# Optimization experiments

Measured on AMD Instinct MI355X. Metric: run time of the kernel, lower is better.

The kernel has to match this reference:

```python
import jax, jax.numpy as jnp
import numpy as np

N = 30000
E = 480000
D = 128
H = 3  # n_hop
BN_EPS = 1e-5


def _bn(x, g, b, m, v):
    # inference-mode BatchNorm1d
    return (x - m) * jax.lax.rsqrt(v + BN_EPS) * g + b


def setup_inputs() -> dict:
    key = jax.random.key(0)
    ks = jax.random.split(key, 16)
    inp = {
        "xs": jax.random.normal(ks[0], (H + 1, N, D), dtype=jnp.float32),
        "ei": jax.random.randint(ks[1], (H, 2, E), 0, N, dtype=jnp.int32),
        "lW1": jax.random.normal(ks[2], (D, D), dtype=jnp.float32) * 0.05,
        "lb1": jnp.zeros((D,), jnp.float32),
        "lg": jax.random.uniform(ks[3], (D,), jnp.float32, 0.5, 1.5),
        "lbt": jax.random.normal(ks[4], (D,), dtype=jnp.float32) * 0.1,
        "lm": jax.random.normal(ks[5], (D,), dtype=jnp.float32) * 0.1,
        "lv": jax.random.uniform(ks[6], (D,), jnp.float32, 0.5, 1.5),
        "lW2": jax.random.normal(ks[7], (D, D), dtype=jnp.float32) * 0.05,
        "lb2": jnp.zeros((D,), jnp.float32),
        "eps": jnp.zeros((H,), jnp.float32),
        "cW1": jax.random.normal(ks[8], (H, D, D), dtype=jnp.float32) * 0.05,
        "cb1": jnp.zeros((H, D), jnp.float32),
        "cg": jax.random.uniform(ks[9], (H, D), jnp.float32, 0.5, 1.5),
        "cbt": jax.random.normal(ks[10], (H, D), dtype=jnp.float32) * 0.1,
        "cm": jax.random.normal(ks[11], (H, D), dtype=jnp.float32) * 0.1,
        "cv": jax.random.uniform(ks[12], (H, D), jnp.float32, 0.5, 1.5),
        "cW2": jax.random.normal(ks[13], (H, D, D), dtype=jnp.float32) * 0.05,
        "cb2": jnp.zeros((H, D), jnp.float32),
    }
    return inp


def reference(xs, ei, lW1, lb1, lg, lbt, lm, lv, lW2, lb2,
              eps, cW1, cb1, cg, cbt, cm, cv, cW2, cb2):
    # self.lin: Linear -> BN -> ReLU -> Linear on multi_input[0]
    h0 = jax.nn.relu(_bn(xs[0] @ lW1 + lb1, lg, lbt, lm, lv)) @ lW2 + lb2
    hidden = h0  # dropout identity (eval)
    for k in range(H):
        x = xs[k + 1]                       # [N, D]
        src, dst = ei[k, 0], ei[k, 1]
        agg = jax.ops.segment_sum(x[src], dst, num_segments=N)  # sum_{j->i} x_j
        z = (1.0 + eps[k]) * x + agg        # GIN update
        prop = jax.nn.relu(_bn(z @ cW1[k] + cb1[k], cg[k], cbt[k], cm[k], cv[k])) @ cW2[k] + cb2[k]
        hidden = hidden + prop
    return hidden
```

## Files before the change

kernel.cpp:

```cpp
#include <hip/hip_runtime.h>

#define N_NODES 30000
#define N_EDGES 480000
#define D 128
#define H 3
#define BN_EPS 1e-5f
#define M_TOT (H * N_NODES)
#define E_TOT (H * N_EDGES)

#define NCH 64
#define CHE (N_EDGES / NCH)
#define NBKT 512
#define NBKT_TOT (H * NBKT)
#define CELLS (NBKT_TOT * NCH)
#define SCAN_NBLK (CELLS / 1024)
#define CONV_N4 (3 * N_NODES * D / 4)
#define CONV_BLK ((CONV_N4 + 255) / 256)
#define TILES ((N_NODES + 63) / 64)
#define PREP_FIX (H * NCH + 9)

typedef __attribute__((ext_vector_type(8))) short short8v;
typedef __attribute__((ext_vector_type(4))) float f32x4;

__device__ __forceinline__ ushort f2bf(float f) {
    uint u = __float_as_uint(f);
    u += 0x7fffu + ((u >> 16) & 1u);
    return (ushort)(u >> 16);
}
__device__ __forceinline__ float bf2f(ushort b) {
    return __uint_as_float(((uint)b) << 16);
}

#define DOT2(accv, w, msk) \
    asm("v_dot2_f32_bf16 %0, %1, %2, %0" : "+v"(accv) : "v"(w), "v"(msk))

__global__ __launch_bounds__(256) void prep_k(
    const float* __restrict__ xs, const int* __restrict__ ei,
    const float* __restrict__ lW1, const float* __restrict__ lW2,
    const float* __restrict__ cW1, const float* __restrict__ cW2,
    const float* __restrict__ lb1, const float* __restrict__ lg,
    const float* __restrict__ lbt, const float* __restrict__ lm,
    const float* __restrict__ lv,
    const float* __restrict__ cb1, const float* __restrict__ cg,
    const float* __restrict__ cbt, const float* __restrict__ cm,
    const float* __restrict__ cv,
    const float* __restrict__ lb2, const float* __restrict__ cb2,
    ushort* __restrict__ Wt, float* __restrict__ scof,
    ushort* __restrict__ xball, int* __restrict__ cnts)
{
    const int bid = blockIdx.x;
    const int tid = threadIdx.x;
    if (bid < H * NCH) {
        __shared__ int hc[NBKT];
        const int hop = bid >> 6, c = bid & 63;
        for (int i = tid; i < NBKT; i += 256) hc[i] = 0;
        __syncthreads();
        const int* dstp = ei + (size_t)hop * 2 * N_EDGES + N_EDGES + c * CHE;
        for (int i = tid; i < CHE; i += 256)
            atomicAdd(&hc[dstp[i] >> 6], 1);
        __syncthreads();
        for (int b = tid; b < NBKT; b += 256)
            cnts[((hop * NBKT + b) << 6) | c] = hc[b];
    } else if (bid < H * NCH + 8) {
        const int mat = bid - H * NCH;
        const float* src;
        if (mat == 0) src = lW1;
        else if (mat == 1) src = lW2;
        else {
            const int k = (mat - 2) >> 1;
            src = ((mat & 1) == 0 ? cW1 : cW2) + (size_t)k * D * D;
        }
        ushort* dst = Wt + (size_t)mat * D * D;
        for (int idx = tid; idx < D * D; idx += 256) {
            const int n = idx >> 7, k = idx & 127;
            dst[idx] = f2bf(src[k * D + n]);
        }
    } else if (bid == H * NCH + 8) {
        for (int t = tid; t < 512; t += 256) {
            const int L = t >> 7, c = t & 127;
            float g, v, b, m, bt;
            if (L == 0) { g = lg[c]; v = lv[c]; b = lb1[c]; m = lm[c]; bt = lbt[c]; }
            else {
                const int k = L - 1;
                g = cg[k * D + c]; v = cv[k * D + c]; b = cb1[k * D + c];
                m = cm[k * D + c]; bt = cbt[k * D + c];
            }
            const float s = g * rsqrtf(v + BN_EPS);
            scof[L * 256 + c] = s;
            scof[L * 256 + 128 + c] = (b - m) * s + bt;
        }
        if (tid < 128) {
            float t = lb2[tid];
            for (int k = 0; k < H; ++k) t += cb2[k * D + tid];
            scof[1024 + tid] = t;
        }
    } else {
        const int i = (bid - PREP_FIX) * 256 + tid;
        if (i < CONV_N4) {
            const float4 v = ((const float4*)(xs + (size_t)N_NODES * D))[i];
            ushort4 o;
            o.x = f2bf(v.x); o.y = f2bf(v.y); o.z = f2bf(v.z); o.w = f2bf(v.w);
            ((ushort4*)(xball + (size_t)N_NODES * D))[i] = o;
        }
    }
}

#define LW 136

__global__ __launch_bounds__(256) void layerpar_k(
    const float* __restrict__ xs0, const ushort* __restrict__ zb,
    const ushort* __restrict__ Wt, const float* __restrict__ scof,
    ushort* __restrict__ parts)
{
    __shared__ ushort Xs[64 * LW];
    __shared__ ushort Ws[128 * LW];
    const int L = blockIdx.x & 3, tile = blockIdx.x >> 2;
    const int row0 = tile * 64;
    const int tid = threadIdx.x;
    const int wave = tid >> 6, lane = tid & 63;
    const int m16 = lane & 15, kq = lane >> 4;

    const ushort* W1t = Wt + (size_t)(2 * L) * D * D;
    const ushort* W2t = W1t + D * D;
    const float* scL = scof + L * 256;

    if (L == 0) {
        for (int f = tid; f < 2048; f += 256) {
            const int r = f >> 5, c4 = (f & 31) << 2;
            const int gr = row0 + r;
            ushort4 v = make_ushort4(0, 0, 0, 0);
            if (gr < N_NODES) {
                const float4 fv = *(const float4*)(xs0 + (size_t)gr * D + c4);
                v.x = f2bf(fv.x); v.y = f2bf(fv.y);
                v.z = f2bf(fv.z); v.w = f2bf(fv.w);
            }
            *(ushort4*)(&Xs[r * LW + c4]) = v;
        }
    } else {
        const ushort* X = zb + (size_t)(L - 1) * N_NODES * D;
        for (int f = tid; f < 2048; f += 256) {
            const int r = f >> 5, c4 = (f & 31) << 2;
            const int gr = row0 + r;
            ushort4 v = make_ushort4(0, 0, 0, 0);
            if (gr < N_NODES) v = *(const ushort4*)(X + (size_t)gr * D + c4);
            *(ushort4*)(&Xs[r * LW + c4]) = v;
        }
    }
    for (int f = tid; f < 4096; f += 256) {
        const int n = f >> 5, c4 = (f & 31) << 2;
        *(ushort4*)(&Ws[n * LW + c4]) = *(const ushort4*)(W1t + n * D + c4);
    }
    __syncthreads();

    const int arow = wave * 16 + m16;
    short8v a[4];
#pragma unroll
    for (int kk = 0; kk < 4; ++kk)
        a[kk] = *(const short8v*)(&Xs[arow * LW + kk * 32 + kq * 8]);

    f32x4 acc[8];
#pragma unroll
    for (int t = 0; t < 8; ++t) acc[t] = (f32x4){0.f, 0.f, 0.f, 0.f};
#pragma unroll
    for (int kk = 0; kk < 4; ++kk) {
#pragma unroll
        for (int t = 0; t < 8; ++t) {
            const short8v b = *(const short8v*)(&Ws[(t * 16 + m16) * LW + kk * 32 + kq * 8]);
            acc[t] = __builtin_amdgcn_mfma_f32_16x16x32_bf16(a[kk], b, acc[t], 0, 0, 0);
        }
    }
    __syncthreads();

#pragma unroll
    for (int t = 0; t < 8; ++t) {
        const int n = t * 16 + m16;
        const float sc = scL[n], of = scL[128 + n];
#pragma unroll
        for (int r = 0; r < 4; ++r)
            Xs[(wave * 16 + kq * 4 + r) * LW + n] = f2bf(fmaxf(acc[t][r] * sc + of, 0.f));
    }
    for (int f = tid; f < 4096; f += 256) {
        const int n = f >> 5, c4 = (f & 31) << 2;
        *(ushort4*)(&Ws[n * LW + c4]) = *(const ushort4*)(W2t + n * D + c4);
    }
    __syncthreads();

    short8v ah[4];
#pragma unroll
    for (int kk = 0; kk < 4; ++kk)
        ah[kk] = *(const short8v*)(&Xs[arow * LW + kk * 32 + kq * 8]);
    f32x4 accO[8];
#pragma unroll
    for (int t = 0; t < 8; ++t) accO[t] = (f32x4){0.f, 0.f, 0.f, 0.f};
#pragma unroll
    for (int kk = 0; kk < 4; ++kk) {
#pragma unroll
        for (int t = 0; t < 8; ++t) {
            const short8v b = *(const short8v*)(&Ws[(t * 16 + m16) * LW + kk * 32 + kq * 8]);
            accO[t] = __builtin_amdgcn_mfma_f32_16x16x32_bf16(ah[kk], b, accO[t], 0, 0, 0);
        }
    }

    ushort* pL = parts + (size_t)L * N_NODES * D;
#pragma unroll
    for (int t = 0; t < 8; ++t) {
        const int n = t * 16 + m16;
#pragma unroll
        for (int r = 0; r < 4; ++r) {
            const int gr = row0 + wave * 16 + kq * 4 + r;
            if (gr < N_NODES) pL[(size_t)gr * D + n] = f2bf(accO[t][r]);
        }
    }
}

__global__ __launch_bounds__(256) void reduce_k(const ushort* __restrict__ parts,
                                                const float* __restrict__ scof,
                                                float* __restrict__ out)
{
    const int i = blockIdx.x * 256 + threadIdx.x;
    const size_t LS = (size_t)N_NODES * D / 4;
    const uint2* pp = (const uint2*)parts;
    const uint2 q0 = pp[i];
    const uint2 q1 = pp[i + LS];
    const uint2 q2 = pp[i + 2 * LS];
    const uint2 q3 = pp[i + 3 * LS];
    const float4 bb = ((const float4*)(scof + 1024))[i & 31];
    float4 s;
    s.x = ((bf2f((ushort)(q0.x & 0xffff)) + bf2f((ushort)(q1.x & 0xffff))) +
           (bf2f((ushort)(q2.x & 0xffff)) + bf2f((ushort)(q3.x & 0xffff)))) + bb.x;
    s.y = ((bf2f((ushort)(q0.x >> 16)) + bf2f((ushort)(q1.x >> 16))) +
           (bf2f((ushort)(q2.x >> 16)) + bf2f((ushort)(q3.x >> 16)))) + bb.y;
    s.z = ((bf2f((ushort)(q0.y & 0xffff)) + bf2f((ushort)(q1.y & 0xffff))) +
           (bf2f((ushort)(q2.y & 0xffff)) + bf2f((ushort)(q3.y & 0xffff)))) + bb.z;
    s.w = ((bf2f((ushort)(q0.y >> 16)) + bf2f((ushort)(q1.y >> 16))) +
           (bf2f((ushort)(q2.y >> 16)) + bf2f((ushort)(q3.y >> 16)))) + bb.w;
    ((float4*)out)[i] = s;
}

__global__ __launch_bounds__(1024) void scanA_k(int* __restrict__ cnts,
                                                int* __restrict__ bsums) {
    __shared__ int sh[1024];
    const int tid = threadIdx.x;
    const int i = blockIdx.x * 1024 + tid;
    const int v = cnts[i];
    sh[tid] = v;
    __syncthreads();
    int val = v;
    for (int off = 1; off < 1024; off <<= 1) {
        const int t = (tid >= off) ? sh[tid - off] : 0;
        __syncthreads();
        val += t;
        sh[tid] = val;
        __syncthreads();
    }
    cnts[i] = val - v;
    if (tid == 1023) bsums[blockIdx.x] = val;
}

__global__ __launch_bounds__(1024) void scanC_k(int* __restrict__ cnts,
                                                const int* __restrict__ bsums,
                                                int* __restrict__ offs) {
    __shared__ int bs[128];
    const int tid = threadIdx.x;
    if (tid < 128) bs[tid] = (tid < SCAN_NBLK) ? bsums[tid] : 0;
    __syncthreads();
    for (int off = 1; off < 128; off <<= 1) {
        int t = 0;
        if (tid < 128 && tid >= off) t = bs[tid - off];
        __syncthreads();
        if (tid < 128) bs[tid] += t;
        __syncthreads();
    }
    const int add = (blockIdx.x == 0) ? 0 : bs[blockIdx.x - 1];
    const int i = blockIdx.x * 1024 + tid;
    cnts[i] += add;
    if (i == 0) offs[M_TOT] = E_TOT;
}

__global__ __launch_bounds__(256) void binplace_k(const int* __restrict__ ei,
                                                  const int* __restrict__ cnts,
                                                  uint* __restrict__ binned) {
    __shared__ int cur[NBKT];
    const int chunk = blockIdx.x;
    const int hop = chunk >> 6, c = chunk & 63;
    for (int b = threadIdx.x; b < NBKT; b += 256)
        cur[b] = cnts[((hop * NBKT + b) << 6) | c];
    __syncthreads();
    const int* srcp = ei + (size_t)hop * 2 * N_EDGES + c * CHE;
    const int* dstp = srcp + N_EDGES;
    for (int i = threadIdx.x; i < CHE; i += 256) {
        const int s = srcp[i], d = dstp[i];
        const int slot = atomicAdd(&cur[d >> 6], 1);
        binned[slot] = ((uint)(d & 63) << 16) | (uint)s;
    }
}

__global__ __launch_bounds__(256) void cat_k(const uint* __restrict__ binned,
                                             const int* __restrict__ cnts,
                                             int* __restrict__ offs,
                                             ushort* __restrict__ srcs) {
    const int B = blockIdx.x;
    const int hop = B >> 9, bb = B & 511;
    const int dstbase = bb << 6;
    if (dstbase >= N_NODES) return;
    const int bB = cnts[B << 6];
    const int bE = (B == NBKT_TOT - 1) ? E_TOT : cnts[(B + 1) << 6];
    const int cnt = bE - bB;

    __shared__ uint ent[2048];
    __shared__ ushort stg[2048];
    __shared__ int hist[64], cur[64];

    for (int d = threadIdx.x; d < 64; d += 256) hist[d] = 0;
    __syncthreads();
    for (int i = threadIdx.x; i < cnt; i += 256) {
        const uint e = binned[bB + i];
        ent[i] = e;
        atomicAdd(&hist[e >> 16], 1);
    }
    __syncthreads();
    if (threadIdx.x < 64) {
        const int v = hist[threadIdx.x];
        int x = v;
        for (int off = 1; off < 64; off <<= 1) {
            const int t = __shfl_up(x, off, 64);
            if (threadIdx.x >= off) x += t;
        }
        cur[threadIdx.x] = x - v;
        const int gd = dstbase + threadIdx.x;
        if (gd < N_NODES) offs[hop * N_NODES + gd] = bB + x - v;
    }
    __syncthreads();
    for (int i = threadIdx.x; i < cnt; i += 256) {
        const uint e = ent[i];
        const int lp = atomicAdd(&cur[e >> 16], 1);
        stg[lp] = (ushort)(e & 0xffffu);
    }
    __syncthreads();
    for (int i = threadIdx.x; i < cnt; i += 256)
        srcs[bB + i] = stg[i];
}

__global__ __launch_bounds__(256) void agg_k(const ushort* __restrict__ xball,
                                             const int* __restrict__ offs,
                                             const ushort* __restrict__ srcs,
                                             const float* __restrict__ eps,
                                             ushort* __restrict__ zb) {
    const int gnode = blockIdx.x * 4 + (threadIdx.x >> 6);
    const int hop = gnode / N_NODES;
    const int node = gnode - hop * N_NODES;
    const int lane = threadIdx.x & 63;
    const int eh = lane >> 4;
    const int cl = lane & 15;
    const float a = 1.0f + eps[hop];
    const char* xb = (const char*)(xball + (size_t)(hop + 1) * N_NODES * D);
    const uint coff = (uint)cl << 4;
    const uint MLO = 0x00003F80u;
    const uint MHI = 0x3F800000u;

    float acc[8];
#pragma unroll
    for (int q = 0; q < 8; ++q) acc[q] = 0.f;
    if (eh == 0) {
        const uint4 sv = *(const uint4*)(xb + (((uint)node << 8) + coff));
        const uint w[4] = {sv.x, sv.y, sv.z, sv.w};
#pragma unroll
        for (int q = 0; q < 4; ++q) {
            acc[2 * q]     = a * bf2f((ushort)(w[q] & 0xffff));
            acc[2 * q + 1] = a * bf2f((ushort)(w[q] >> 16));
        }
    }

    const int beg = offs[gnode], end = offs[gnode + 1];
    for (int i = beg; i < end; i += 32) {
        uint4 v[8];
#pragma unroll
        for (int u = 0; u < 8; ++u) {
            const int p = i + u * 4 + eh;
            v[u] = make_uint4(0u, 0u, 0u, 0u);
            if (p < end) {
                const uint boff = ((uint)srcs[p] << 8) + coff;
                v[u] = *(const uint4*)(xb + boff);
            }
        }
#pragma unroll
        for (int u = 0; u < 8; ++u) {
            DOT2(acc[0], v[u].x, MLO); DOT2(acc[1], v[u].x, MHI);
            DOT2(acc[2], v[u].y, MLO); DOT2(acc[3], v[u].y, MHI);
            DOT2(acc[4], v[u].z, MLO); DOT2(acc[5], v[u].z, MHI);
            DOT2(acc[6], v[u].w, MLO); DOT2(acc[7], v[u].w, MHI);
        }
    }
#pragma unroll
    for (int q = 0; q < 8; ++q) {
        acc[q] += __shfl_xor(acc[q], 16);
        acc[q] += __shfl_xor(acc[q], 32);
    }
    if (eh == 0) {
        uint4 o;
        o.x = (uint)f2bf(acc[0]) | ((uint)f2bf(acc[1]) << 16);
        o.y = (uint)f2bf(acc[2]) | ((uint)f2bf(acc[3]) << 16);
        o.z = (uint)f2bf(acc[4]) | ((uint)f2bf(acc[5]) << 16);
        o.w = (uint)f2bf(acc[6]) | ((uint)f2bf(acc[7]) << 16);
        ((uint4*)zb)[(size_t)gnode * 16 + cl] = o;
    }
}

extern "C" void kernel_launch(void* const* d_in, const int* in_sizes, int n_in,
                              void* d_out, int out_size, void* d_ws, size_t ws_size,
                              hipStream_t stream)
{
    const float* xs  = (const float*)d_in[0];
    const int*   ei  = (const int*)d_in[1];
    const float* lW1 = (const float*)d_in[2];
    const float* lb1 = (const float*)d_in[3];
    const float* lg  = (const float*)d_in[4];
    const float* lbt = (const float*)d_in[5];
    const float* lm  = (const float*)d_in[6];
    const float* lv  = (const float*)d_in[7];
    const float* lW2 = (const float*)d_in[8];
    const float* lb2 = (const float*)d_in[9];
    const float* eps = (const float*)d_in[10];
    const float* cW1 = (const float*)d_in[11];
    const float* cb1 = (const float*)d_in[12];
    const float* cg  = (const float*)d_in[13];
    const float* cbt = (const float*)d_in[14];
    const float* cm  = (const float*)d_in[15];
    const float* cv  = (const float*)d_in[16];
    const float* cW2 = (const float*)d_in[17];
    const float* cb2 = (const float*)d_in[18];
    float* out = (float*)d_out;

    char* ws = (char*)d_ws;
    ushort* xball = (ushort*)ws; ws += (size_t)4 * N_NODES * D * sizeof(ushort);
    ushort* zb    = (ushort*)ws; ws += (size_t)H * N_NODES * D * sizeof(ushort);
    ushort* parts = (ushort*)ws; ws += (size_t)4 * N_NODES * D * sizeof(ushort);
    ushort* Wt    = (ushort*)ws; ws += (size_t)8 * D * D * sizeof(ushort);
    float*  scof  = (float*)ws;  ws += (size_t)(4 * 256 + 128) * sizeof(float);
    int* cnts     = (int*)ws;    ws += (size_t)CELLS * sizeof(int);
    int* bsums    = (int*)ws;    ws += 128 * sizeof(int);
    int* offs     = (int*)ws;    ws += (size_t)(M_TOT + 64) * sizeof(int);
    uint* binned  = (uint*)ws;   ws += (size_t)E_TOT * sizeof(uint);
    ushort* srcs  = (ushort*)ws;

    prep_k<<<PREP_FIX + CONV_BLK, 256, 0, stream>>>(
        xs, ei, lW1, lW2, cW1, cW2, lb1, lg, lbt, lm, lv,
        cb1, cg, cbt, cm, cv, lb2, cb2, Wt, scof, xball, cnts);

    scanA_k<<<SCAN_NBLK, 1024, 0, stream>>>(cnts, bsums);
    scanC_k<<<SCAN_NBLK, 1024, 0, stream>>>(cnts, bsums, offs);
    binplace_k<<<H * NCH, 256, 0, stream>>>(ei, cnts, binned);
    cat_k<<<NBKT_TOT, 256, 0, stream>>>(binned, cnts, offs, srcs);

    agg_k<<<M_TOT / 4, 256, 0, stream>>>(xball, offs, srcs, eps, zb);
    layerpar_k<<<TILES * 4, 256, 0, stream>>>(xs, zb, Wt, scof, parts);
    reduce_k<<<(N_NODES * D / 4) / 256, 256, 0, stream>>>(parts, scof, out);
}
```

Before: 155.6 us.

## Fuse second-layer GEMMs into one K=512 GEMM replacing partial sums and reduce

The four per-layer second linear layers and the reduction kernel are replaced by one concatenated GEMM. The hidden activations of all four branches are stored side by side as an [N,512] bf16 matrix, and the W2 matrices are concatenated along K, so a single GEMM with the combined bias gives the output directly. This removes the bf16 partial buffers, their extra rounding and the separate reduce pass. The first GEMM kernel also drops LDS staging and reads operands straight from global memory, which saves barriers but relies on cache hits for the repeated W1 fragment loads.

Result: slower. 187.5 us (+20.5%).

```diff
diff --git a/kernel.cpp b/kernel.cpp
--- a/kernel.cpp
+++ b/kernel.cpp
@@ -17,7 +17,8 @@
 #define CONV_N4 (3 * N_NODES * D / 4)
 #define CONV_BLK ((CONV_N4 + 255) / 256)
 #define TILES ((N_NODES + 63) / 64)
-#define PREP_FIX (H * NCH + 9)
+#define PREP_FIX (H * NCH + 13)
+#define DK 512
 
 typedef __attribute__((ext_vector_type(8))) short short8v;
 typedef __attribute__((ext_vector_type(4))) float f32x4;
@@ -46,7 +47,8 @@
     const float* __restrict__ cv,
     const float* __restrict__ lb2, const float* __restrict__ cb2,
     ushort* __restrict__ Wt, float* __restrict__ scof,
-    ushort* __restrict__ xball, int* __restrict__ cnts)
+    ushort* __restrict__ xball, int* __restrict__ cnts,
+    ushort* __restrict__ W2c)
 {
     const int bid = blockIdx.x;
     const int tid = threadIdx.x;
@@ -94,6 +96,13 @@
             for (int k = 0; k < H; ++k) t += cb2[k * D + tid];
             scof[1024 + tid] = t;
         }
+    } else if (bid < H * NCH + 13) {
+        const int L = bid - (H * NCH + 9);
+        const float* src = (L == 0) ? lW2 : cW2 + (size_t)(L - 1) * D * D;
+        for (int idx = tid; idx < D * D; idx += 256) {
+            const int n = idx >> 7, k = idx & 127;
+            W2c[(size_t)n * DK + L * D + k] = f2bf(src[k * D + n]);
+        }
     } else {
         const int i = (bid - PREP_FIX) * 256 + tid;
         if (i < CONV_N4) {
@@ -105,136 +114,116 @@
     }
 }
 
-#define LW 136
-
-__global__ __launch_bounds__(256) void layerpar_k(
+__global__ __launch_bounds__(256) void hgen_k(
     const float* __restrict__ xs0, const ushort* __restrict__ zb,
     const ushort* __restrict__ Wt, const float* __restrict__ scof,
-    ushort* __restrict__ parts)
+    ushort* __restrict__ Hm)
 {
-    __shared__ ushort Xs[64 * LW];
-    __shared__ ushort Ws[128 * LW];
     const int L = blockIdx.x & 3, tile = blockIdx.x >> 2;
-    const int row0 = tile * 64;
-    const int tid = threadIdx.x;
-    const int wave = tid >> 6, lane = tid & 63;
+    const int wave = threadIdx.x >> 6, lane = threadIdx.x & 63;
     const int m16 = lane & 15, kq = lane >> 4;
+    const int rbase = tile * 64 + wave * 16;
+    const int arow = rbase + m16;
 
     const ushort* W1t = Wt + (size_t)(2 * L) * D * D;
-    const ushort* W2t = W1t + D * D;
     const float* scL = scof + L * 256;
 
+    short8v a[4];
     if (L == 0) {
-        for (int f = tid; f < 2048; f += 256) {
-            const int r = f >> 5, c4 = (f & 31) << 2;
-            const int gr = row0 + r;
-            ushort4 v = make_ushort4(0, 0, 0, 0);
-            if (gr < N_NODES) {
-                const float4 fv = *(const float4*)(xs0 + (size_t)gr * D + c4);
-                v.x = f2bf(fv.x); v.y = f2bf(fv.y);
-                v.z = f2bf(fv.z); v.w = f2bf(fv.w);
+        if (arow < N_NODES) {
+            const float* xp = xs0 + (size_t)arow * D + kq * 8;
+#pragma unroll
+            for (int kk = 0; kk < 4; ++kk) {
+                const float4 f0 = *(const float4*)(xp + kk * 32);
+                const float4 f1 = *(const float4*)(xp + kk * 32 + 4);
+                short8v av;
+                av[0] = (short)f2bf(f0.x); av[1] = (short)f2bf(f0.y);
+                av[2] = (short)f2bf(f0.z); av[3] = (short)f2bf(f0.w);
+                av[4] = (short)f2bf(f1.x); av[5] = (short)f2bf(f1.y);
+                av[6] = (short)f2bf(f1.z); av[7] = (short)f2bf(f1.w);
+                a[kk] = av;
             }
-            *(ushort4*)(&Xs[r * LW + c4]) = v;
+        } else {
+#pragma unroll
+            for (int kk = 0; kk < 4; ++kk) a[kk] = (short8v)(short)0;
         }
     } else {
-        const ushort* X = zb + (size_t)(L - 1) * N_NODES * D;
-        for (int f = tid; f < 2048; f += 256) {
-            const int r = f >> 5, c4 = (f & 31) << 2;
-            const int gr = row0 + r;
-            ushort4 v = make_ushort4(0, 0, 0, 0);
-            if (gr < N_NODES) v = *(const ushort4*)(X + (size_t)gr * D + c4);
-            *(ushort4*)(&Xs[r * LW + c4]) = v;
-        }
-    }
-    for (int f = tid; f < 4096; f += 256) {
-        const int n = f >> 5, c4 = (f & 31) << 2;
-        *(ushort4*)(&Ws[n * LW + c4]) = *(const ushort4*)(W1t + n * D + c4);
-    }
-    __syncthreads();
-
-    const int arow = wave * 16 + m16;
-    short8v a[4];
-#pragma unroll
-    for (int kk = 0; kk < 4; ++kk)
-        a[kk] = *(const short8v*)(&Xs[arow * LW + kk * 32 + kq * 8]);
+        if (arow < N_NODES) {
+            const ushort* xp = zb + (size_t)(L - 1) * N_NODES * D
+                                  + (size_t)arow * D + kq * 8;
+#pragma unroll
+            for (int kk = 0; kk < 4; ++kk)
+                a[kk] = *(const short8v*)(xp + kk * 32);
+        } else {
+#pragma unroll
+            for (int kk = 0; kk < 4; ++kk) a[kk] = (short8v)(short)0;
+        }
+    }
 
     f32x4 acc[8];
 #pragma unroll
     for (int t = 0; t < 8; ++t) acc[t] = (f32x4){0.f, 0.f, 0.f, 0.f};
 #pragma unroll
     for (int kk = 0; kk < 4; ++kk) {
-#pragma unroll
-        for (int t = 0; t < 8; ++t) {
-            const short8v b = *(const short8v*)(&Ws[(t * 16 + m16) * LW + kk * 32 + kq * 8]);
-            acc[t] = __builtin_amdgcn_mfma_f32_16x16x32_bf16(a[kk], b, acc[t], 0, 0, 0);
-        }
-    }
-    __syncthreads();
+        short8v bfr[8];
+#pragma unroll
+        for (int t = 0; t < 8; ++t)
+            bfr[t] = *(const short8v*)(W1t + (t * 16 + m16) * D + kk * 32 + kq * 8);
+#pragma unroll
+        for (int t = 0; t < 8; ++t)
+            acc[t] = __builtin_amdgcn_mfma_f32_16x16x32_bf16(a[kk], bfr[t], acc[t], 0, 0, 0);
+    }
 
 #pragma unroll
     for (int t = 0; t < 8; ++t) {
         const int n = t * 16 + m16;
         const float sc = scL[n], of = scL[128 + n];
 #pragma unroll
+        for (int r = 0; r < 4; ++r) {
+            const int gr = rbase + kq * 4 + r;
+            if (gr < N_NODES)
+                Hm[(size_t)gr * DK + L * D + n] = f2bf(fmaxf(acc[t][r] * sc + of, 0.f));
+        }
+    }
+}
+
+__global__ __launch_bounds__(256) void gemm2_k(
+    const ushort* __restrict__ Hm, const ushort* __restrict__ W2c,
+    const float* __restrict__ scof, float* __restrict__ out)
+{
+    const int gid = blockIdx.x * 4 + (threadIdx.x >> 6);
+    const int mt = gid >> 1, nh = gid & 1;
+    if (mt >= N_NODES / 16) return;
+    const int lane = threadIdx.x & 63;
+    const int m16 = lane & 15, kq = lane >> 4;
+    const int r0 = mt * 16;
+    const ushort* hp = Hm + (size_t)(r0 + m16) * DK + kq * 8;
+
+    f32x4 acc[4];
+#pragma unroll
+    for (int t = 0; t < 4; ++t) acc[t] = (f32x4){0.f, 0.f, 0.f, 0.f};
+
+#pragma unroll
+    for (int kk = 0; kk < 16; ++kk) {
+        const short8v a = *(const short8v*)(hp + kk * 32);
+        short8v bfr[4];
+#pragma unroll
+        for (int t = 0; t < 4; ++t)
+            bfr[t] = *(const short8v*)(W2c + (size_t)(nh * 64 + t * 16 + m16) * DK + kk * 32 + kq * 8);
+#pragma unroll
+        for (int t = 0; t < 4; ++t)
+            acc[t] = __builtin_amdgcn_mfma_f32_16x16x32_bf16(a, bfr[t], acc[t], 0, 0, 0);
+    }
+
+    const float* btot = scof + 1024;
+#pragma unroll
+    for (int t = 0; t < 4; ++t) {
+        const int n = nh * 64 + t * 16 + m16;
+        const float bb = btot[n];
+#pragma unroll
         for (int r = 0; r < 4; ++r)
-            Xs[(wave * 16 + kq * 4 + r) * LW + n] = f2bf(fmaxf(acc[t][r] * sc + of, 0.f));
-    }
-    for (int f = tid; f < 4096; f += 256) {
-        const int n = f >> 5, c4 = (f & 31) << 2;
-        *(ushort4*)(&Ws[n * LW + c4]) = *(const ushort4*)(W2t + n * D + c4);
-    }
-    __syncthreads();
-
-    short8v ah[4];
-#pragma unroll
-    for (int kk = 0; kk < 4; ++kk)
-        ah[kk] = *(const short8v*)(&Xs[arow * LW + kk * 32 + kq * 8]);
-    f32x4 accO[8];
-#pragma unroll
-    for (int t = 0; t < 8; ++t) accO[t] = (f32x4){0.f, 0.f, 0.f, 0.f};
-#pragma unroll
-    for (int kk = 0; kk < 4; ++kk) {
-#pragma unroll
-        for (int t = 0; t < 8; ++t) {
-            const short8v b = *(const short8v*)(&Ws[(t * 16 + m16) * LW + kk * 32 + kq * 8]);
-            accO[t] = __builtin_amdgcn_mfma_f32_16x16x32_bf16(ah[kk], b, accO[t], 0, 0, 0);
-        }
-    }
-
-    ushort* pL = parts + (size_t)L * N_NODES * D;
-#pragma unroll
-    for (int t = 0; t < 8; ++t) {
-        const int n = t * 16 + m16;
-#pragma unroll
-        for (int r = 0; r < 4; ++r) {
-            const int gr = row0 + wave * 16 + kq * 4 + r;
-            if (gr < N_NODES) pL[(size_t)gr * D + n] = f2bf(accO[t][r]);
-        }
-    }
-}
-
-__global__ __launch_bounds__(256) void reduce_k(const ushort* __restrict__ parts,
-                                                const float* __restrict__ scof,
-                                                float* __restrict__ out)
-{
-    const int i = blockIdx.x * 256 + threadIdx.x;
-    const size_t LS = (size_t)N_NODES * D / 4;
-    const uint2* pp = (const uint2*)parts;
-    const uint2 q0 = pp[i];
-    const uint2 q1 = pp[i + LS];
-    const uint2 q2 = pp[i + 2 * LS];
-    const uint2 q3 = pp[i + 3 * LS];
-    const float4 bb = ((const float4*)(scof + 1024))[i & 31];
-    float4 s;
-    s.x = ((bf2f((ushort)(q0.x & 0xffff)) + bf2f((ushort)(q1.x & 0xffff))) +
-           (bf2f((ushort)(q2.x & 0xffff)) + bf2f((ushort)(q3.x & 0xffff)))) + bb.x;
-    s.y = ((bf2f((ushort)(q0.x >> 16)) + bf2f((ushort)(q1.x >> 16))) +
-           (bf2f((ushort)(q2.x >> 16)) + bf2f((ushort)(q3.x >> 16)))) + bb.y;
-    s.z = ((bf2f((ushort)(q0.y & 0xffff)) + bf2f((ushort)(q1.y & 0xffff))) +
-           (bf2f((ushort)(q2.y & 0xffff)) + bf2f((ushort)(q3.y & 0xffff)))) + bb.z;
-    s.w = ((bf2f((ushort)(q0.y >> 16)) + bf2f((ushort)(q1.y >> 16))) +
-           (bf2f((ushort)(q2.y >> 16)) + bf2f((ushort)(q3.y >> 16)))) + bb.w;
-    ((float4*)out)[i] = s;
+            out[(size_t)(r0 + kq * 4 + r) * D + n] = acc[t][r] + bb;
+    }
 }
 
 __global__ __launch_bounds__(1024) void scanA_k(int* __restrict__ cnts,
@@ -434,8 +423,9 @@
     char* ws = (char*)d_ws;
     ushort* xball = (ushort*)ws; ws += (size_t)4 * N_NODES * D * sizeof(ushort);
     ushort* zb    = (ushort*)ws; ws += (size_t)H * N_NODES * D * sizeof(ushort);
-    ushort* parts = (ushort*)ws; ws += (size_t)4 * N_NODES * D * sizeof(ushort);
+    ushort* Hm    = (ushort*)ws; ws += (size_t)N_NODES * DK * sizeof(ushort);
     ushort* Wt    = (ushort*)ws; ws += (size_t)8 * D * D * sizeof(ushort);
+    ushort* W2c   = (ushort*)ws; ws += (size_t)D * DK * sizeof(ushort);
     float*  scof  = (float*)ws;  ws += (size_t)(4 * 256 + 128) * sizeof(float);
     int* cnts     = (int*)ws;    ws += (size_t)CELLS * sizeof(int);
     int* bsums    = (int*)ws;    ws += 128 * sizeof(int);
@@ -445,7 +435,7 @@
 
     prep_k<<<PREP_FIX + CONV_BLK, 256, 0, stream>>>(
         xs, ei, lW1, lW2, cW1, cW2, lb1, lg, lbt, lm, lv,
-        cb1, cg, cbt, cm, cv, lb2, cb2, Wt, scof, xball, cnts);
+        cb1, cg, cbt, cm, cv, lb2, cb2, Wt, scof, xball, cnts, W2c);
 
     scanA_k<<<SCAN_NBLK, 1024, 0, stream>>>(cnts, bsums);
     scanC_k<<<SCAN_NBLK, 1024, 0, stream>>>(cnts, bsums, offs);
@@ -453,6 +443,6 @@
     cat_k<<<NBKT_TOT, 256, 0, stream>>>(binned, cnts, offs, srcs);
 
     agg_k<<<M_TOT / 4, 256, 0, stream>>>(xball, offs, srcs, eps, zb);
-    layerpar_k<<<TILES * 4, 256, 0, stream>>>(xs, zb, Wt, scof, parts);
-    reduce_k<<<(N_NODES * D / 4) / 256, 256, 0, stream>>>(parts, scof, out);
-}
+    hgen_k<<<TILES * 4, 256, 0, stream>>>(xs, zb, Wt, scof, Hm);
+    gemm2_k<<<(N_NODES / 16 * 2 + 3) / 4, 256, 0, stream>>>(Hm, W2c, scof, out);
+}
```

## Use XOR-swizzled LDS layout with direct global-to-LDS loads in layer GEMM

Applied to the files above, without the earlier changes.

Replaces the padded LDS rows in the layer MLP kernel with an XOR-swizzled unpadded layout and has producers (weight transpose, hop-0 bf16 conversion, aggregation output) write data pre-swizzled. Tiles are then loaded with global_load_lds directly into LDS, both weight matrices are staged up front, and one of the barriers is dropped. Hop-0 features are now converted to bf16 in the prep kernel instead of inside the GEMM. This aims to cut register round-trips and barrier stalls, at the cost of more LDS per block, which may lower occupancy. The last partial tile's loads are no longer bounds-checked, so they can read past the row count.

Measured after the change: 137.3 us. -11.7%, faster.

```diff
diff --git a/kernel.cpp b/kernel.cpp
--- a/kernel.cpp
+++ b/kernel.cpp
@@ -17,6 +17,7 @@
 #define CONV_N4 (3 * N_NODES * D / 4)
 #define CONV_BLK ((CONV_N4 + 255) / 256)
 #define TILES ((N_NODES + 63) / 64)
+#define S0_BLK (N_NODES * 16 / 256)
 #define PREP_FIX (H * NCH + 9)
 
 typedef __attribute__((ext_vector_type(8))) short short8v;
@@ -33,6 +34,12 @@
 
 #define DOT2(accv, w, msk) \
     asm("v_dot2_f32_bf16 %0, %1, %2, %0" : "+v"(accv) : "v"(w), "v"(msk))
+
+__device__ __forceinline__ void gload16(const void* g, void* l) {
+    __builtin_amdgcn_global_load_lds(
+        (const __attribute__((address_space(1))) void*)g,
+        (__attribute__((address_space(3))) void*)l, 16, 0, 0);
+}
 
 __global__ __launch_bounds__(256) void prep_k(
     const float* __restrict__ xs, const int* __restrict__ ei,
@@ -73,7 +80,7 @@
         ushort* dst = Wt + (size_t)mat * D * D;
         for (int idx = tid; idx < D * D; idx += 256) {
             const int n = idx >> 7, k = idx & 127;
-            dst[idx] = f2bf(src[k * D + n]);
+            dst[n * 128 + (k ^ ((n & 7) << 3))] = f2bf(src[k * D + n]);
         }
     } else if (bid == H * NCH + 8) {
         for (int t = tid; t < 512; t += 256) {
@@ -94,8 +101,20 @@
             for (int k = 0; k < H; ++k) t += cb2[k * D + tid];
             scof[1024 + tid] = t;
         }
+    } else if (bid < PREP_FIX + S0_BLK) {
+        const int i = (bid - PREP_FIX) * 256 + tid;
+        const int row = i >> 4, c = i & 15;
+        const float* sp = xs + (size_t)row * D + c * 8;
+        const float4 f0 = ((const float4*)sp)[0];
+        const float4 f1 = ((const float4*)sp)[1];
+        uint4 o;
+        o.x = (uint)f2bf(f0.x) | ((uint)f2bf(f0.y) << 16);
+        o.y = (uint)f2bf(f0.z) | ((uint)f2bf(f0.w) << 16);
+        o.z = (uint)f2bf(f1.x) | ((uint)f2bf(f1.y) << 16);
+        o.w = (uint)f2bf(f1.z) | ((uint)f2bf(f1.w) << 16);
+        ((uint4*)xball)[(size_t)row * 16 + (c ^ (row & 7))] = o;
     } else {
-        const int i = (bid - PREP_FIX) * 256 + tid;
+        const int i = (bid - PREP_FIX - S0_BLK) * 256 + tid;
         if (i < CONV_N4) {
             const float4 v = ((const float4*)(xs + (size_t)N_NODES * D))[i];
             ushort4 o;
@@ -105,15 +124,14 @@
     }
 }
 
-#define LW 136
-
 __global__ __launch_bounds__(256) void layerpar_k(
-    const float* __restrict__ xs0, const ushort* __restrict__ zb,
+    const ushort* __restrict__ xball, const ushort* __restrict__ zb,
     const ushort* __restrict__ Wt, const float* __restrict__ scof,
     ushort* __restrict__ parts)
 {
-    __shared__ ushort Xs[64 * LW];
-    __shared__ ushort Ws[128 * LW];
+    __shared__ ushort Xs[64 * 128];
+    __shared__ ushort Ws1[128 * 128];
+    __shared__ ushort Ws2[128 * 128];
     const int L = blockIdx.x & 3, tile = blockIdx.x >> 2;
     const int row0 = tile * 64;
     const int tid = threadIdx.x;
@@ -122,41 +140,28 @@
 
     const ushort* W1t = Wt + (size_t)(2 * L) * D * D;
     const ushort* W2t = W1t + D * D;
+    const ushort* Xsrc = (L == 0) ? xball : zb + (size_t)(L - 1) * N_NODES * D;
     const float* scL = scof + L * 256;
 
-    if (L == 0) {
-        for (int f = tid; f < 2048; f += 256) {
-            const int r = f >> 5, c4 = (f & 31) << 2;
-            const int gr = row0 + r;
-            ushort4 v = make_ushort4(0, 0, 0, 0);
-            if (gr < N_NODES) {
-                const float4 fv = *(const float4*)(xs0 + (size_t)gr * D + c4);
-                v.x = f2bf(fv.x); v.y = f2bf(fv.y);
-                v.z = f2bf(fv.z); v.w = f2bf(fv.w);
-            }
-            *(ushort4*)(&Xs[r * LW + c4]) = v;
-        }
-    } else {
-        const ushort* X = zb + (size_t)(L - 1) * N_NODES * D;
-        for (int f = tid; f < 2048; f += 256) {
-            const int r = f >> 5, c4 = (f & 31) << 2;
-            const int gr = row0 + r;
-            ushort4 v = make_ushort4(0, 0, 0, 0);
-            if (gr < N_NODES) v = *(const ushort4*)(X + (size_t)gr * D + c4);
-            *(ushort4*)(&Xs[r * LW + c4]) = v;
-        }
-    }
-    for (int f = tid; f < 4096; f += 256) {
-        const int n = f >> 5, c4 = (f & 31) << 2;
-        *(ushort4*)(&Ws[n * LW + c4]) = *(const ushort4*)(W1t + n * D + c4);
-    }
-    __syncthreads();
-
-    const int arow = wave * 16 + m16;
+#pragma unroll
+    for (int it = 0; it < 4; ++it) {
+        const int r = wave * 16 + it * 4;
+        gload16(Xsrc + (size_t)(row0 + r) * 128 + lane * 8, &Xs[r * 128]);
+    }
+#pragma unroll
+    for (int it = 0; it < 8; ++it) {
+        const int r = wave * 32 + it * 4;
+        gload16(W1t + (size_t)r * 128 + lane * 8, &Ws1[r * 128]);
+        gload16(W2t + (size_t)r * 128 + lane * 8, &Ws2[r * 128]);
+    }
+    __syncthreads();
+
+    const int sx = (m16 & 7) << 3;
+
     short8v a[4];
 #pragma unroll
     for (int kk = 0; kk < 4; ++kk)
-        a[kk] = *(const short8v*)(&Xs[arow * LW + kk * 32 + kq * 8]);
+        a[kk] = *(const short8v*)(&Xs[(wave * 16 + m16) * 128 + ((kk * 32 + kq * 8) ^ sx)]);
 
     f32x4 acc[8];
 #pragma unroll
@@ -165,30 +170,27 @@
     for (int kk = 0; kk < 4; ++kk) {
 #pragma unroll
         for (int t = 0; t < 8; ++t) {
-            const short8v b = *(const short8v*)(&Ws[(t * 16 + m16) * LW + kk * 32 + kq * 8]);
+            const short8v b = *(const short8v*)(&Ws1[(t * 16 + m16) * 128 + ((kk * 32 + kq * 8) ^ sx)]);
             acc[t] = __builtin_amdgcn_mfma_f32_16x16x32_bf16(a[kk], b, acc[t], 0, 0, 0);
         }
     }
-    __syncthreads();
 
 #pragma unroll
     for (int t = 0; t < 8; ++t) {
         const int n = t * 16 + m16;
         const float sc = scL[n], of = scL[128 + n];
 #pragma unroll
-        for (int r = 0; r < 4; ++r)
-            Xs[(wave * 16 + kq * 4 + r) * LW + n] = f2bf(fmaxf(acc[t][r] * sc + of, 0.f));
-    }
-    for (int f = tid; f < 4096; f += 256) {
-        const int n = f >> 5, c4 = (f & 31) << 2;
-        *(ushort4*)(&Ws[n * LW + c4]) = *(const ushort4*)(W2t + n * D + c4);
-    }
-    __syncthreads();
+        for (int r = 0; r < 4; ++r) {
+            const int ml = wave * 16 + kq * 4 + r;
+            Xs[ml * 128 + (n ^ (((kq * 4 + r) & 7) << 3))] =
+                f2bf(fmaxf(acc[t][r] * sc + of, 0.f));
+        }
+    }
 
     short8v ah[4];
 #pragma unroll
     for (int kk = 0; kk < 4; ++kk)
-        ah[kk] = *(const short8v*)(&Xs[arow * LW + kk * 32 + kq * 8]);
+        ah[kk] = *(const short8v*)(&Xs[(wave * 16 + m16) * 128 + ((kk * 32 + kq * 8) ^ sx)]);
     f32x4 accO[8];
 #pragma unroll
     for (int t = 0; t < 8; ++t) accO[t] = (f32x4){0.f, 0.f, 0.f, 0.f};
@@ -196,7 +198,7 @@
     for (int kk = 0; kk < 4; ++kk) {
 #pragma unroll
         for (int t = 0; t < 8; ++t) {
-            const short8v b = *(const short8v*)(&Ws[(t * 16 + m16) * LW + kk * 32 + kq * 8]);
+            const short8v b = *(const short8v*)(&Ws2[(t * 16 + m16) * 128 + ((kk * 32 + kq * 8) ^ sx)]);
             accO[t] = __builtin_amdgcn_mfma_f32_16x16x32_bf16(ah[kk], b, accO[t], 0, 0, 0);
         }
     }
@@ -402,7 +404,7 @@
         o.y = (uint)f2bf(acc[2]) | ((uint)f2bf(acc[3]) << 16);
         o.z = (uint)f2bf(acc[4]) | ((uint)f2bf(acc[5]) << 16);
         o.w = (uint)f2bf(acc[6]) | ((uint)f2bf(acc[7]) << 16);
-        ((uint4*)zb)[(size_t)gnode * 16 + cl] = o;
+        ((uint4*)zb)[(size_t)gnode * 16 + (cl ^ (gnode & 7))] = o;
     }
 }
 
@@ -443,7 +445,7 @@
     uint* binned  = (uint*)ws;   ws += (size_t)E_TOT * sizeof(uint);
     ushort* srcs  = (ushort*)ws;
 
-    prep_k<<<PREP_FIX + CONV_BLK, 256, 0, stream>>>(
+    prep_k<<<PREP_FIX + S0_BLK + CONV_BLK, 256, 0, stream>>>(
         xs, ei, lW1, lW2, cW1, cW2, lb1, lg, lbt, lm, lv,
         cb1, cg, cbt, cm, cv, lb2, cb2, Wt, scof, xball, cnts);
 
@@ -453,6 +455,6 @@
     cat_k<<<NBKT_TOT, 256, 0, stream>>>(binned, cnts, offs, srcs);
 
     agg_k<<<M_TOT / 4, 256, 0, stream>>>(xball, offs, srcs, eps, zb);
-    layerpar_k<<<TILES * 4, 256, 0, stream>>>(xs, zb, Wt, scof, parts);
+    layerpar_k<<<TILES * 4, 256, 0, stream>>>(xball, zb, Wt, scof, parts);
     reduce_k<<<(N_NODES * D / 4) / 256, 256, 0, stream>>>(parts, scof, out);
 }
```
